# Optimization experiments

Hardware: AMD Instinct MI355X
Metric: run time of the kernel (lower is better)

The kernel has to match this reference:

```python
import jax, jax.numpy as jnp
import numpy as np

M = 4096        # node_num
NN = 16         # neighbors per node (nn_num)
G = 4           # graph_num
IN_F = 32
OUT_F = 32
LOC_F = 8
LHID = 128
B = 16


def setup_inputs() -> dict:
    key = jax.random.key(0)
    ks = jax.random.split(key, 9)
    return {
        "x": jax.random.normal(ks[0], (B, M, IN_F), jnp.float32),
        "maps": jax.random.normal(ks[1], (M * NN, LOC_F), jnp.float32),
        "L_idx": jax.random.randint(ks[2], (M * NN,), 0, M * M, jnp.int64 if jax.config.jax_enable_x64 else jnp.int32),
        "W1": jax.random.normal(ks[3], (G, LHID, LOC_F), jnp.float32) * 0.1,
        "b1": jax.random.normal(ks[4], (G, LHID), jnp.float32) * 0.1,
        "W2": jax.random.normal(ks[5], (G, LHID), jnp.float32) * 0.1,
        "b2": jax.random.normal(ks[6], (G,), jnp.float32) * 0.1,
        "Wx": jax.random.normal(ks[7], (G, IN_F, OUT_F), jnp.float32) * 0.1,
        "bx": jax.random.normal(ks[8], (OUT_F,), jnp.float32) * 0.1,
    }


def reference(x, maps, L_idx, W1, b1, W2, b2, Wx, bx):
    # x: (B, m, in_f); maps: (m*nn, loc); L_idx: (m*nn,) indices into flat m*m
    g, lhid, loc = W1.shape
    bsz, m, f = x.shape
    nn_num = maps.shape[0] // m

    # per-graph tiny MLP over all node-neighbor pairs, vectorized over graphs
    h = jnp.tanh(jnp.einsum("nl,ghl->gnh", maps, W1) + b1[:, None, :])   # (g, m*nn, lhid)
    ctx = jnp.einsum("gnh,gh->gn", h, W2) + b2[:, None]                   # (g, m*nn)
    # softmax over the nn_num neighbors of each node (F.softmax on (m, nn) -> dim=1)
    attn = jax.nn.softmax(ctx.reshape(g, m, nn_num), axis=-1).reshape(g, m * nn_num)

    # scatter attention into dense per-graph Laplacians: L[L_idx] = attn
    L = jnp.zeros((g, m * m), attn.dtype).at[:, L_idx].set(attn).reshape(g, m, m)

    # XeLayer: out = sum_g (L_g @ x) @ Wx_g + bx
    agg = jnp.einsum("gij,bjf->gbif", L, x)          # (g, B, m, f)
    out = jnp.einsum("gbif,gfo->bio", agg, Wx) + bx   # (B, m, out_f)
    return out
```

## Files before the change

### kernel.cpp

```cpp
#include <hip/hip_runtime.h>

#define M_NODES 4096
#define NN_NUM 16
#define G_NUM 4
#define IN_F 32
#define OUT_F 32
#define LOC_F 8
#define LHID 128
#define B_SZ 16
#define NPAIR 65536
#define ROWCAP 64

typedef __attribute__((ext_vector_type(8))) short short8;
typedef __attribute__((ext_vector_type(4))) float f32x4;

static __device__ __forceinline__ unsigned short f2bf(float f) {
  union { float f; unsigned u; } c; c.f = f;
  const unsigned r = c.u + 0x7FFFu + ((c.u >> 16) & 1u);
  return (unsigned short)(r >> 16);
}
static __device__ __forceinline__ float bfhi2f(unsigned u) {
  union { unsigned u; float f; } c; c.u = u & 0xFFFF0000u; return c.f;
}
static __device__ __forceinline__ float bflo2f(unsigned u) {
  union { unsigned u; float f; } c; c.u = u << 16; return c.f;
}

__global__ void __launch_bounds__(256)
prep_kernel(const float4* __restrict__ x4,
            const float* __restrict__ maps,
            const float* __restrict__ W1,
            const float* __restrict__ b1,
            const float* __restrict__ W2,
            const float* __restrict__ Wx,
            ushort4* __restrict__ xb4,
            uint4* __restrict__ mapsbf4,
            ushort* __restrict__ w1bf,
            float2* __restrict__ b1w2,
            ushort4* __restrict__ wxf4,
            unsigned* __restrict__ rowcount) {
  const int idx = blockIdx.x * 256 + threadIdx.x;

#pragma unroll
  for (int k = 0; k < 2; ++k) {
    const float4 v = x4[idx + k * 262144];
    ushort4 o;
    o.x = f2bf(v.x); o.y = f2bf(v.y); o.z = f2bf(v.z); o.w = f2bf(v.w);
    xb4[idx + k * 262144] = o;
  }

  if (idx < NPAIR) {
    const float4 a = *reinterpret_cast<const float4*>(maps + (size_t)idx * 8);
    const float4 b = *reinterpret_cast<const float4*>(maps + (size_t)idx * 8 + 4);
    uint4 r;
    r.x = (unsigned)f2bf(a.x) | ((unsigned)f2bf(a.y) << 16);
    r.y = (unsigned)f2bf(a.z) | ((unsigned)f2bf(a.w) << 16);
    r.z = (unsigned)f2bf(b.x) | ((unsigned)f2bf(b.y) << 16);
    r.w = (unsigned)f2bf(b.z) | ((unsigned)f2bf(b.w) << 16);
    mapsbf4[idx] = r;
  }

  if (idx < G_NUM * LHID * LOC_F) w1bf[idx] = f2bf(W1[idx]);
  if (idx < G_NUM * LHID)
    b1w2[idx] = make_float2(b1[idx], W2[idx]);

  if (idx < 512) {
    const int l = idx & 63, tile = (idx >> 6) & 1, g = idx >> 7;
    const int lo = l & 15, hi = l >> 4;
    ushort4 r0, r1;
    r0.x = f2bf(Wx[g * 1024 + (hi * 8 + 0) * 32 + tile * 16 + lo]);
    r0.y = f2bf(Wx[g * 1024 + (hi * 8 + 1) * 32 + tile * 16 + lo]);
    r0.z = f2bf(Wx[g * 1024 + (hi * 8 + 2) * 32 + tile * 16 + lo]);
    r0.w = f2bf(Wx[g * 1024 + (hi * 8 + 3) * 32 + tile * 16 + lo]);
    r1.x = f2bf(Wx[g * 1024 + (hi * 8 + 4) * 32 + tile * 16 + lo]);
    r1.y = f2bf(Wx[g * 1024 + (hi * 8 + 5) * 32 + tile * 16 + lo]);
    r1.z = f2bf(Wx[g * 1024 + (hi * 8 + 6) * 32 + tile * 16 + lo]);
    r1.w = f2bf(Wx[g * 1024 + (hi * 8 + 7) * 32 + tile * 16 + lo]);
    wxf4[idx * 2] = r0;
    wxf4[idx * 2 + 1] = r1;
  }

  if (idx < M_NODES) rowcount[idx] = 0;
}

__global__ void __launch_bounds__(256)
mlp_kernel(const ushort* __restrict__ mapsbf,
           const ushort* __restrict__ w1bf,
           const float2* __restrict__ b1w2,
           const int* __restrict__ L_idx,
           unsigned* __restrict__ rowcount,
           uint2* __restrict__ csr_jn,
           float4* __restrict__ csr_a) {
  const int t = threadIdx.x;
  const int l = t & 63;
  const int g = t >> 6;
  const int node = blockIdx.x;
  const int lo = l & 15;
  const int hi = l >> 4;

  __shared__ float sAttn[G_NUM][16];

  short8 aF = {0, 0, 0, 0, 0, 0, 0, 0};
  if (hi == 0)
    aF = *reinterpret_cast<const short8*>(mapsbf + ((size_t)node * 16 + lo) * 8);

  short8 bF[8];
  float2 bw[8];
#pragma unroll
  for (int tile = 0; tile < 8; ++tile) {
    bF[tile] = *reinterpret_cast<const short8*>(
        w1bf + ((size_t)(g * LHID + tile * 16 + lo)) * 8);
    bw[tile] = b1w2[g * LHID + tile * 16 + lo];
  }

  float cr[4] = {0.f, 0.f, 0.f, 0.f};
#pragma unroll
  for (int tile = 0; tile < 8; ++tile) {
    const float b1v = bw[tile].x;
    const float w2h = bw[tile].y;
    f32x4 c = {b1v, b1v, b1v, b1v};
    c = __builtin_amdgcn_mfma_f32_16x16x32_bf16(aF, bF[tile], c, 0, 0, 0);
#pragma unroll
    for (int r = 0; r < 4; ++r) {
      const float h = c[r];
      const float tt = h * h;
      const float num = h * (15.0f + tt);
      const float den = fmaf(6.0f, tt, 15.0f);
      cr[r] = fmaf(w2h, num * __builtin_amdgcn_rcpf(den), cr[r]);
    }
  }

#pragma unroll
  for (int m = 1; m <= 8; m <<= 1) {
    cr[0] += __shfl_xor(cr[0], m, 64);
    cr[1] += __shfl_xor(cr[1], m, 64);
    cr[2] += __shfl_xor(cr[2], m, 64);
    cr[3] += __shfl_xor(cr[3], m, 64);
  }

  float mx = fmaxf(fmaxf(cr[0], cr[1]), fmaxf(cr[2], cr[3]));
  mx = fmaxf(mx, __shfl_xor(mx, 16, 64));
  mx = fmaxf(mx, __shfl_xor(mx, 32, 64));
  const float e0 = __expf(cr[0] - mx), e1 = __expf(cr[1] - mx);
  const float e2 = __expf(cr[2] - mx), e3 = __expf(cr[3] - mx);
  float s = e0 + e1 + e2 + e3;
  s += __shfl_xor(s, 16, 64);
  s += __shfl_xor(s, 32, 64);
  const float inv = __builtin_amdgcn_rcpf(s);

  if (lo == 0) {
    sAttn[g][hi * 4 + 0] = e0 * inv;
    sAttn[g][hi * 4 + 1] = e1 * inv;
    sAttn[g][hi * 4 + 2] = e2 * inv;
    sAttn[g][hi * 4 + 3] = e3 * inv;
  }
  __syncthreads();

  if (t < 16) {
    const int n = node * 16 + t;
    const unsigned pos = (unsigned)L_idx[n];
    const unsigned i = pos >> 12;
    const unsigned j = pos & (M_NODES - 1);
    const unsigned slot = atomicAdd(&rowcount[i], 1u);
    if (slot < ROWCAP) {
      csr_jn[(size_t)i * ROWCAP + slot] = make_uint2(j, (unsigned)n);
      csr_a[(size_t)i * ROWCAP + slot] =
          make_float4(sAttn[0][t], sAttn[1][t], sAttn[2][t], sAttn[3][t]);
    }
  }
}

__global__ void __launch_bounds__(256)
gather_kernel(const ushort* __restrict__ xbf,
              const uint2* __restrict__ csr_jn,
              const float4* __restrict__ csr_a,
              const unsigned* __restrict__ rowcount,
              const ushort* __restrict__ wxf,
              const float* __restrict__ bx,
              float* __restrict__ out) {
  const int t = threadIdx.x;
  const int l = t & 63;
  const int i = blockIdx.x * 4 + (t >> 6);
  const int lo = l & 15;
  const int hi = l >> 4;

  short8 bF[G_NUM][2];
#pragma unroll
  for (int g = 0; g < G_NUM; ++g)
#pragma unroll
    for (int tile = 0; tile < 2; ++tile)
      bF[g][tile] = *reinterpret_cast<const short8*>(
          wxf + ((size_t)((g * 2 + tile) * 64 + l)) * 8);

  const unsigned cnt = min(rowcount[i], (unsigned)ROWCAP);
  const uint2 e = csr_jn[(size_t)i * ROWCAP + l];
  float4 aq = csr_a[(size_t)i * ROWCAP + l];
  const bool valid = (unsigned)l < cnt;
  unsigned myj = valid ? e.x : 0xFFFFFFFFu;
  const unsigned myn = valid ? e.y : 0u;

  bool alive = valid;
  for (unsigned d = 0; d < cnt; ++d) {
    const unsigned jd = __shfl(myj, (int)d);
    const unsigned nd = __shfl(myn, (int)d);
    if (jd == myj && nd > myn) alive = false;
  }
  if (!alive) { aq.x = 0.f; aq.y = 0.f; aq.z = 0.f; aq.w = 0.f; }
  myj &= (M_NODES - 1u);

  float acc[G_NUM][8];
#pragma unroll
  for (int g = 0; g < G_NUM; ++g)
#pragma unroll
    for (int q = 0; q < 8; ++q) acc[g][q] = 0.f;

  const uint4* xrow = reinterpret_cast<const uint4*>(xbf) + hi;
  const size_t browbase = (size_t)lo * M_NODES * 4;

  for (unsigned s = 0; s < cnt; ++s) {
    const unsigned js = __shfl(myj, (int)s);
    const float w0 = __shfl(aq.x, (int)s);
    const float w1 = __shfl(aq.y, (int)s);
    const float w2 = __shfl(aq.z, (int)s);
    const float w3 = __shfl(aq.w, (int)s);
    const uint4 xv = xrow[browbase + (size_t)js * 4];
    float xf[8];
    xf[0] = bflo2f(xv.x); xf[1] = bfhi2f(xv.x);
    xf[2] = bflo2f(xv.y); xf[3] = bfhi2f(xv.y);
    xf[4] = bflo2f(xv.z); xf[5] = bfhi2f(xv.z);
    xf[6] = bflo2f(xv.w); xf[7] = bfhi2f(xv.w);
#pragma unroll
    for (int q = 0; q < 8; ++q) {
      acc[0][q] = fmaf(w0, xf[q], acc[0][q]);
      acc[1][q] = fmaf(w1, xf[q], acc[1][q]);
      acc[2][q] = fmaf(w2, xf[q], acc[2][q]);
      acc[3][q] = fmaf(w3, xf[q], acc[3][q]);
    }
  }

  f32x4 c0 = {0.f, 0.f, 0.f, 0.f};
  f32x4 c1 = {0.f, 0.f, 0.f, 0.f};
#pragma unroll
  for (int g = 0; g < G_NUM; ++g) {
    short8 aF;
#pragma unroll
    for (int q = 0; q < 8; ++q) aF[q] = (short)f2bf(acc[g][q]);
    c0 = __builtin_amdgcn_mfma_f32_16x16x32_bf16(aF, bF[g][0], c0, 0, 0, 0);
    c1 = __builtin_amdgcn_mfma_f32_16x16x32_bf16(aF, bF[g][1], c1, 0, 0, 0);
  }

  const float bias0 = bx[lo];
  const float bias1 = bx[16 + lo];
#pragma unroll
  for (int r = 0; r < 4; ++r) {
    const int b = hi * 4 + r;
    float* op = out + ((size_t)b * M_NODES + i) * OUT_F;
    op[lo] = c0[r] + bias0;
    op[16 + lo] = c1[r] + bias1;
  }
}

extern "C" void kernel_launch(void* const* d_in, const int* in_sizes, int n_in,
                              void* d_out, int out_size, void* d_ws, size_t ws_size,
                              hipStream_t stream) {
  const float* x    = (const float*)d_in[0];
  const float* maps = (const float*)d_in[1];
  const int*   L_idx = (const int*)d_in[2];
  const float* W1   = (const float*)d_in[3];
  const float* b1   = (const float*)d_in[4];
  const float* W2   = (const float*)d_in[5];
  const float* Wx   = (const float*)d_in[7];
  const float* bx   = (const float*)d_in[8];
  float* out = (float*)d_out;

  char* ws = (char*)d_ws;
  float4*   csr_a    = (float4*)ws;
  uint2*    csr_jn   = (uint2*)(ws + (4u << 20));
  ushort*   xbf      = (ushort*)(ws + (6u << 20));
  unsigned* rowcount = (unsigned*)(ws + (10u << 20));
  ushort*   mapsbf   = (ushort*)(ws + (11u << 20));
  ushort*   w1bf     = (ushort*)(ws + (12u << 20));
  float2*   b1w2     = (float2*)(ws + (12u << 20) + (32u << 10));
  ushort*   wxf      = (ushort*)(ws + (12u << 20) + (64u << 10));

  prep_kernel<<<1024, 256, 0, stream>>>(
      (const float4*)x, maps, W1, b1, W2, Wx,
      (ushort4*)xbf, (uint4*)mapsbf, w1bf, b1w2, (ushort4*)wxf, rowcount);
  mlp_kernel<<<M_NODES, 256, 0, stream>>>(
      mapsbf, w1bf, b1w2, L_idx, rowcount, csr_jn, csr_a);
  gather_kernel<<<M_NODES / 4, 256, 0, stream>>>(
      xbf, csr_jn, csr_a, rowcount, wxf, bx, out);
}
```

Baseline: 42.35 us.

## Fold prep kernel into MLP kernel and zero row counts with memset

Removes the separate prep kernel. Bf16 conversion of maps, W1, b1/W2 now happens inline in the MLP kernel, Wx conversion is done by block 0, and the x-to-bf16 conversion is spread across all MLP blocks after the scatter. Row counters are zeroed with an async memset instead. This saves a kernel launch and the intermediate bf16 buffers, but each block now redundantly converts W1 from fp32, and a memset node is added.

```diff
diff --git a/kernel.cpp b/kernel.cpp
--- a/kernel.cpp
+++ b/kernel.cpp
@@ -27,67 +27,15 @@
 }
 
 __global__ void __launch_bounds__(256)
-prep_kernel(const float4* __restrict__ x4,
-            const float* __restrict__ maps,
-            const float* __restrict__ W1,
-            const float* __restrict__ b1,
-            const float* __restrict__ W2,
-            const float* __restrict__ Wx,
-            ushort4* __restrict__ xb4,
-            uint4* __restrict__ mapsbf4,
-            ushort* __restrict__ w1bf,
-            float2* __restrict__ b1w2,
-            ushort4* __restrict__ wxf4,
-            unsigned* __restrict__ rowcount) {
-  const int idx = blockIdx.x * 256 + threadIdx.x;
-
-#pragma unroll
-  for (int k = 0; k < 2; ++k) {
-    const float4 v = x4[idx + k * 262144];
-    ushort4 o;
-    o.x = f2bf(v.x); o.y = f2bf(v.y); o.z = f2bf(v.z); o.w = f2bf(v.w);
-    xb4[idx + k * 262144] = o;
-  }
-
-  if (idx < NPAIR) {
-    const float4 a = *reinterpret_cast<const float4*>(maps + (size_t)idx * 8);
-    const float4 b = *reinterpret_cast<const float4*>(maps + (size_t)idx * 8 + 4);
-    uint4 r;
-    r.x = (unsigned)f2bf(a.x) | ((unsigned)f2bf(a.y) << 16);
-    r.y = (unsigned)f2bf(a.z) | ((unsigned)f2bf(a.w) << 16);
-    r.z = (unsigned)f2bf(b.x) | ((unsigned)f2bf(b.y) << 16);
-    r.w = (unsigned)f2bf(b.z) | ((unsigned)f2bf(b.w) << 16);
-    mapsbf4[idx] = r;
-  }
-
-  if (idx < G_NUM * LHID * LOC_F) w1bf[idx] = f2bf(W1[idx]);
-  if (idx < G_NUM * LHID)
-    b1w2[idx] = make_float2(b1[idx], W2[idx]);
-
-  if (idx < 512) {
-    const int l = idx & 63, tile = (idx >> 6) & 1, g = idx >> 7;
-    const int lo = l & 15, hi = l >> 4;
-    ushort4 r0, r1;
-    r0.x = f2bf(Wx[g * 1024 + (hi * 8 + 0) * 32 + tile * 16 + lo]);
-    r0.y = f2bf(Wx[g * 1024 + (hi * 8 + 1) * 32 + tile * 16 + lo]);
-    r0.z = f2bf(Wx[g * 1024 + (hi * 8 + 2) * 32 + tile * 16 + lo]);
-    r0.w = f2bf(Wx[g * 1024 + (hi * 8 + 3) * 32 + tile * 16 + lo]);
-    r1.x = f2bf(Wx[g * 1024 + (hi * 8 + 4) * 32 + tile * 16 + lo]);
-    r1.y = f2bf(Wx[g * 1024 + (hi * 8 + 5) * 32 + tile * 16 + lo]);
-    r1.z = f2bf(Wx[g * 1024 + (hi * 8 + 6) * 32 + tile * 16 + lo]);
-    r1.w = f2bf(Wx[g * 1024 + (hi * 8 + 7) * 32 + tile * 16 + lo]);
-    wxf4[idx * 2] = r0;
-    wxf4[idx * 2 + 1] = r1;
-  }
-
-  if (idx < M_NODES) rowcount[idx] = 0;
-}
-
-__global__ void __launch_bounds__(256)
-mlp_kernel(const ushort* __restrict__ mapsbf,
-           const ushort* __restrict__ w1bf,
-           const float2* __restrict__ b1w2,
+mlp_kernel(const float4* __restrict__ x4,
+           const float* __restrict__ maps,
+           const float* __restrict__ W1,
+           const float* __restrict__ b1,
+           const float* __restrict__ W2,
+           const float* __restrict__ Wx,
            const int* __restrict__ L_idx,
+           ushort4* __restrict__ xb4,
+           ushort4* __restrict__ wxf4,
            unsigned* __restrict__ rowcount,
            uint2* __restrict__ csr_jn,
            float4* __restrict__ csr_a) {
@@ -100,17 +48,50 @@
 
   __shared__ float sAttn[G_NUM][16];
 
+  if (blockIdx.x == 0) {
+    for (int idx = t; idx < 512; idx += 256) {
+      const int fl = idx & 63, tile = (idx >> 6) & 1, fg = idx >> 7;
+      const int flo = fl & 15, fhi = fl >> 4;
+      ushort4 r0, r1;
+      r0.x = f2bf(Wx[fg * 1024 + (fhi * 8 + 0) * 32 + tile * 16 + flo]);
+      r0.y = f2bf(Wx[fg * 1024 + (fhi * 8 + 1) * 32 + tile * 16 + flo]);
+      r0.z = f2bf(Wx[fg * 1024 + (fhi * 8 + 2) * 32 + tile * 16 + flo]);
+      r0.w = f2bf(Wx[fg * 1024 + (fhi * 8 + 3) * 32 + tile * 16 + flo]);
+      r1.x = f2bf(Wx[fg * 1024 + (fhi * 8 + 4) * 32 + tile * 16 + flo]);
+      r1.y = f2bf(Wx[fg * 1024 + (fhi * 8 + 5) * 32 + tile * 16 + flo]);
+      r1.z = f2bf(Wx[fg * 1024 + (fhi * 8 + 6) * 32 + tile * 16 + flo]);
+      r1.w = f2bf(Wx[fg * 1024 + (fhi * 8 + 7) * 32 + tile * 16 + flo]);
+      wxf4[idx * 2] = r0;
+      wxf4[idx * 2 + 1] = r1;
+    }
+  }
+
   short8 aF = {0, 0, 0, 0, 0, 0, 0, 0};
-  if (hi == 0)
-    aF = *reinterpret_cast<const short8*>(mapsbf + ((size_t)node * 16 + lo) * 8);
+  if (hi == 0) {
+    const float4 ma = *reinterpret_cast<const float4*>(
+        maps + ((size_t)node * 16 + lo) * 8);
+    const float4 mb = *reinterpret_cast<const float4*>(
+        maps + ((size_t)node * 16 + lo) * 8 + 4);
+    aF[0] = (short)f2bf(ma.x); aF[1] = (short)f2bf(ma.y);
+    aF[2] = (short)f2bf(ma.z); aF[3] = (short)f2bf(ma.w);
+    aF[4] = (short)f2bf(mb.x); aF[5] = (short)f2bf(mb.y);
+    aF[6] = (short)f2bf(mb.z); aF[7] = (short)f2bf(mb.w);
+  }
 
   short8 bF[8];
   float2 bw[8];
 #pragma unroll
   for (int tile = 0; tile < 8; ++tile) {
-    bF[tile] = *reinterpret_cast<const short8*>(
-        w1bf + ((size_t)(g * LHID + tile * 16 + lo)) * 8);
-    bw[tile] = b1w2[g * LHID + tile * 16 + lo];
+    const int h = g * LHID + tile * 16 + lo;
+    const float4 wa = *reinterpret_cast<const float4*>(W1 + (size_t)h * 8);
+    const float4 wb = *reinterpret_cast<const float4*>(W1 + (size_t)h * 8 + 4);
+    short8 f;
+    f[0] = (short)f2bf(wa.x); f[1] = (short)f2bf(wa.y);
+    f[2] = (short)f2bf(wa.z); f[3] = (short)f2bf(wa.w);
+    f[4] = (short)f2bf(wb.x); f[5] = (short)f2bf(wb.y);
+    f[6] = (short)f2bf(wb.z); f[7] = (short)f2bf(wb.w);
+    bF[tile] = f;
+    bw[tile] = make_float2(b1[h], W2[h]);
   }
 
   float cr[4] = {0.f, 0.f, 0.f, 0.f};
@@ -166,6 +147,17 @@
       csr_jn[(size_t)i * ROWCAP + slot] = make_uint2(j, (unsigned)n);
       csr_a[(size_t)i * ROWCAP + slot] =
           make_float4(sAttn[0][t], sAttn[1][t], sAttn[2][t], sAttn[3][t]);
+    }
+  }
+
+  __builtin_amdgcn_sched_barrier(0);
+  {
+    const int idx = blockIdx.x * 256 + t;
+    if (idx < 524288) {
+      const float4 v = x4[idx];
+      ushort4 o;
+      o.x = f2bf(v.x); o.y = f2bf(v.y); o.z = f2bf(v.z); o.w = f2bf(v.w);
+      xb4[idx] = o;
     }
   }
 }
@@ -278,16 +270,12 @@
   uint2*    csr_jn   = (uint2*)(ws + (4u << 20));
   ushort*   xbf      = (ushort*)(ws + (6u << 20));
   unsigned* rowcount = (unsigned*)(ws + (10u << 20));
-  ushort*   mapsbf   = (ushort*)(ws + (11u << 20));
-  ushort*   w1bf     = (ushort*)(ws + (12u << 20));
-  float2*   b1w2     = (float2*)(ws + (12u << 20) + (32u << 10));
-  ushort*   wxf      = (ushort*)(ws + (12u << 20) + (64u << 10));
-
-  prep_kernel<<<1024, 256, 0, stream>>>(
-      (const float4*)x, maps, W1, b1, W2, Wx,
-      (ushort4*)xbf, (uint4*)mapsbf, w1bf, b1w2, (ushort4*)wxf, rowcount);
+  ushort*   wxf      = (ushort*)(ws + (11u << 20));
+
+  hipMemsetAsync(rowcount, 0, M_NODES * sizeof(unsigned), stream);
   mlp_kernel<<<M_NODES, 256, 0, stream>>>(
-      mapsbf, w1bf, b1w2, L_idx, rowcount, csr_jn, csr_a);
+      (const float4*)x, maps, W1, b1, W2, Wx, L_idx,
+      (ushort4*)xbf, (ushort4*)wxf, rowcount, csr_jn, csr_a);
   gather_kernel<<<M_NODES / 4, 256, 0, stream>>>(
       xbf, csr_jn, csr_a, rowcount, wxf, bx, out);
 }
```

Result: slower. 46.82 us (+10.5%).
